# Kernel optimization log

Measured on AMD Instinct MI355X. Metric: run time of the kernel, lower is better.

The kernel has to match this reference:

```python
import math
import jax, jax.numpy as jnp
import numpy as np

EMBED = 256
HEADS = 8
HEAD_DIM = 32
LAYERS = 6
FFN = 1024
CLAMP = 30
EPS = 1e-12


def _layer_norm(x, g, b):
    m = jnp.mean(x, axis=-1, keepdims=True)
    v = jnp.mean(jnp.square(x - m), axis=-1, keepdims=True)
    return (x - m) * jax.lax.rsqrt(v + EPS) * g + b


def setup_inputs() -> dict:
    key = jax.random.key(0)
    ks = jax.random.split(key, 24)
    B, N = 8, 1023
    S = N + 1
    sd = 0.02
    inp = {}
    inp["node_feat"] = jax.random.normal(ks[0], (B, N, 140), jnp.float32)
    inp["node_opcode"] = jax.random.randint(ks[1], (B, N), 0, 120)
    inp["dist_matrix"] = jax.random.randint(ks[2], (B, S, S), 0, 64)
    # node embedder params
    inp["W_op"] = jax.random.normal(ks[3], (120, EMBED), jnp.float32) * sd
    inp["W_feat"] = jax.random.normal(ks[4], (140, EMBED), jnp.float32) * sd
    inp["b_feat"] = jnp.zeros((EMBED,), jnp.float32)
    inp["W_mlp1"] = jax.random.normal(ks[5], (2 * EMBED, EMBED), jnp.float32) * sd
    inp["b_mlp1"] = jnp.zeros((EMBED,), jnp.float32)
    inp["W_mlp2"] = jax.random.normal(ks[6], (EMBED, EMBED), jnp.float32) * sd
    inp["b_mlp2"] = jnp.zeros((EMBED,), jnp.float32)
    inp["cls"] = jax.random.normal(ks[7], (1, 1, EMBED), jnp.float32)
    # distance bias table: mat[i] = e^(-i/sqrt(clamp)) - 1, size clamp+2
    inp["dist_table"] = jnp.asarray(
        [math.e ** (-i / CLAMP ** 0.5) - 1.0 for i in range(CLAMP + 2)], jnp.float32)
    # transformer layer params, stacked over layers
    inp["Wq"] = jax.random.normal(ks[8], (LAYERS, EMBED, EMBED), jnp.float32) * sd
    inp["bq"] = jnp.zeros((LAYERS, EMBED), jnp.float32)
    inp["Wk"] = jax.random.normal(ks[9], (LAYERS, EMBED, EMBED), jnp.float32) * sd
    inp["bk"] = jnp.zeros((LAYERS, EMBED), jnp.float32)
    inp["Wv"] = jax.random.normal(ks[10], (LAYERS, EMBED, EMBED), jnp.float32) * sd
    inp["bv"] = jnp.zeros((LAYERS, EMBED), jnp.float32)
    inp["Wo"] = jax.random.normal(ks[11], (LAYERS, EMBED, EMBED), jnp.float32) * sd
    inp["bo"] = jnp.zeros((LAYERS, EMBED), jnp.float32)
    inp["ln1_g"] = jnp.ones((LAYERS, EMBED), jnp.float32)
    inp["ln1_b"] = jnp.zeros((LAYERS, EMBED), jnp.float32)
    inp["Wf1"] = jax.random.normal(ks[12], (LAYERS, EMBED, FFN), jnp.float32) * sd
    inp["bf1"] = jnp.zeros((LAYERS, FFN), jnp.float32)
    inp["Wf2"] = jax.random.normal(ks[13], (LAYERS, FFN, EMBED), jnp.float32) * sd
    inp["bf2"] = jnp.zeros((LAYERS, EMBED), jnp.float32)
    inp["ln2_g"] = jnp.ones((LAYERS, EMBED), jnp.float32)
    inp["ln2_b"] = jnp.zeros((LAYERS, EMBED), jnp.float32)
    return inp


def reference(node_feat, W_op, W_feat, b_feat, W_mlp1, b_mlp1, W_mlp2, b_mlp2,
              cls, dist_table, Wq, bq, Wk, bk, Wv, bv, Wo, bo, ln1_g, ln1_b,
              Wf1, bf1, Wf2, bf2, ln2_g, ln2_b, node_opcode, dist_matrix):
    B, N, _ = node_feat.shape
    S = N + 1
    # node embedder: [op_emb ; feat_proj] -> Linear -> GELU -> Linear
    op_enc = W_op[node_opcode]                                  # [B,N,E]
    f_enc = node_feat @ W_feat + b_feat                         # [B,N,E]
    h = jnp.concatenate([op_enc, f_enc], axis=-1)               # [B,N,2E]
    h = jax.nn.gelu(h @ W_mlp1 + b_mlp1, approximate=False) @ W_mlp2 + b_mlp2
    x = jnp.concatenate([jnp.broadcast_to(cls, (B, 1, EMBED)), h], axis=1)  # [B,S,E]
    # distance bias: -1 -> clamp+2, >clamp -> clamp+1, then table gather
    d = dist_matrix
    idx = jnp.where(d == -1, CLAMP + 2, jnp.where(d > CLAMP, CLAMP + 1, d))
    bias = dist_table[idx]                                      # [B,S,S]
    bias4 = bias[:, None, :, :]                                 # broadcast over heads
    scale = 1.0 / math.sqrt(HEAD_DIM)

    def split_heads(t):
        return t.reshape(B, S, HEADS, HEAD_DIM).transpose(0, 2, 1, 3)

    for i in range(LAYERS):
        q = split_heads(x @ Wq[i] + bq[i])                      # [B,H,S,Dh]
        k = split_heads(x @ Wk[i] + bk[i])
        v = split_heads(x @ Wv[i] + bv[i])
        scores = jnp.einsum('bhqd,bhkd->bhqk', q, k) * scale + bias4
        attn = jax.nn.softmax(scores, axis=-1)
        ctx = jnp.einsum('bhqk,bhkd->bhqd', attn, v)
        ctx = ctx.transpose(0, 2, 1, 3).reshape(B, S, EMBED)
        x = _layer_norm(x + ctx @ Wo[i] + bo[i], ln1_g[i], ln1_b[i])
        ff = jax.nn.gelu(x @ Wf1[i] + bf1[i], approximate=False) @ Wf2[i] + bf2[i]
        x = _layer_norm(x + ff, ln2_g[i], ln2_b[i])
    return x
```

## Files before the change

### kernel.cpp

```cpp
#include <hip/hip_runtime.h>
#include <math.h>

#define B_ 8
#define N_ 1023
#define S_ 1024
#define E_ 256
#define H_ 8
#define D_ 32
#define L_ 6
#define F_ 1024
#define LDK 72

typedef __attribute__((ext_vector_type(8))) short bf16x8;
typedef __attribute__((ext_vector_type(4))) float f32x4;

__device__ __forceinline__ ushort f2b(float x) {
    unsigned u = __float_as_uint(x);
    return (ushort)((u + 0x7fffu + ((u >> 16) & 1u)) >> 16);
}

__global__ __launch_bounds__(256) void bias_kernel(const int* __restrict__ dm,
                                                   const float* __restrict__ table,
                                                   float* __restrict__ out) {
    int idx = blockIdx.x * 256 + threadIdx.x;
    int d = dm[idx];
    int ii = ((unsigned)d > 30u) ? 31 : d;
    out[idx] = table[ii];
}

__global__ __launch_bounds__(256) void opgather_kernel(const int* __restrict__ opc,
                                                       const float* __restrict__ W_op,
                                                       float* __restrict__ hcat) {
    int idx = blockIdx.x * 256 + threadIdx.x;
    int row = idx >> 8, c = idx & 255;
    hcat[(size_t)row * 512 + c] = W_op[opc[row] * 256 + c];
}

__global__ __launch_bounds__(256) void assemble_kernel(const float* __restrict__ cls,
                                                       const float* __restrict__ h,
                                                       float* __restrict__ x,
                                                       ushort* __restrict__ xb) {
    int idx = blockIdx.x * 256 + threadIdx.x;
    int c = idx & 255;
    int s = (idx >> 8) & 1023;
    int b = idx >> 18;
    float v = (s == 0) ? cls[c] : h[((size_t)(b * N_ + s - 1)) * 256 + c];
    x[idx] = v;
    xb[idx] = f2b(v);
}

__global__ __launch_bounds__(256) void wconv_t(const float* __restrict__ in,
                                               ushort* __restrict__ out,
                                               int K, int Nn) {
    int idx = blockIdx.x * 256 + threadIdx.x;
    int per = K * Nn;
    int lw = idx / per, rem = idx - lw * per;
    int n = rem / K, k = rem - n * K;
    out[idx] = f2b(in[(size_t)lw * per + (size_t)k * Nn + n]);
}

template<int EPI>
__global__ __launch_bounds__(256) void mgemm(
    const ushort* __restrict__ A, const ushort* __restrict__ Bt,
    const float* __restrict__ bias, void* __restrict__ C,
    int M, int Nn, int K)
{
    __shared__ ushort As[64 * 32];
    __shared__ ushort Bs[64 * 32];
    const int t = threadIdx.x;
    const int m0 = blockIdx.x * 64, n0 = blockIdx.y * 64;
    const int l = t & 63, w = t >> 6;
    const int wr = (w >> 1) * 32, wc = (w & 1) * 32;
    const int sr = t >> 2, sc = (t & 3) * 8;
    const int l15 = l & 15, lk = (l >> 4) * 8;

    f32x4 zero = {0.f, 0.f, 0.f, 0.f};
    f32x4 acc00 = zero, acc01 = zero, acc10 = zero, acc11 = zero;

    const ushort* ap = A + (size_t)(m0 + sr) * K + sc;
    const ushort* bp = Bt + (size_t)(n0 + sr) * K + sc;
    bf16x8 ra = *(const bf16x8*)ap;
    bf16x8 rb = *(const bf16x8*)bp;

    for (int kt = 0; kt < K; kt += 32) {
        *(bf16x8*)&As[sr * 32 + sc] = ra;
        *(bf16x8*)&Bs[sr * 32 + sc] = rb;
        __syncthreads();
        if (kt + 32 < K) {
            ra = *(const bf16x8*)(ap + kt + 32);
            rb = *(const bf16x8*)(bp + kt + 32);
        }
        bf16x8 a0 = *(bf16x8*)&As[(wr + l15) * 32 + lk];
        bf16x8 a1 = *(bf16x8*)&As[(wr + 16 + l15) * 32 + lk];
        bf16x8 b0 = *(bf16x8*)&Bs[(wc + l15) * 32 + lk];
        bf16x8 b1 = *(bf16x8*)&Bs[(wc + 16 + l15) * 32 + lk];
        acc00 = __builtin_amdgcn_mfma_f32_16x16x32_bf16(a0, b0, acc00, 0, 0, 0);
        acc01 = __builtin_amdgcn_mfma_f32_16x16x32_bf16(a0, b1, acc01, 0, 0, 0);
        acc10 = __builtin_amdgcn_mfma_f32_16x16x32_bf16(a1, b0, acc10, 0, 0, 0);
        acc11 = __builtin_amdgcn_mfma_f32_16x16x32_bf16(a1, b1, acc11, 0, 0, 0);
        __syncthreads();
    }
    const int cn = n0 + wc + l15;
    const int rbase = m0 + wr + (l >> 4) * 4;
    float bv0 = bias[cn], bv1 = bias[cn + 16];
    #pragma unroll
    for (int i = 0; i < 2; i++) {
        f32x4 aj0 = i ? acc10 : acc00;
        f32x4 aj1 = i ? acc11 : acc01;
        #pragma unroll
        for (int r = 0; r < 4; r++) {
            int row = rbase + i * 16 + r;
            float v0 = aj0[r] + bv0;
            float v1 = aj1[r] + bv1;
            if (EPI == 0) {
                ((float*)C)[(size_t)row * Nn + cn] = v0;
                ((float*)C)[(size_t)row * Nn + cn + 16] = v1;
            } else {
                if (EPI == 1) {
                    v0 = 0.5f * v0 * (1.f + erff(v0 * 0.70710678118654752f));
                    v1 = 0.5f * v1 * (1.f + erff(v1 * 0.70710678118654752f));
                }
                ((ushort*)C)[(size_t)row * Nn + cn] = f2b(v0);
                ((ushort*)C)[(size_t)row * Nn + cn + 16] = f2b(v1);
            }
        }
    }
}

template<int EPI>
__global__ __launch_bounds__(256) void gemm_kernel(
    const float* __restrict__ A, int lda,
    const float* __restrict__ Bm, int ldb,
    const float* __restrict__ bias,
    float* __restrict__ C, int ldc,
    int M, int Nn, int K)
{
    __shared__ float As[16][68];
    __shared__ float Bs[16][68];
    const int t = threadIdx.x;
    const int m0 = blockIdx.x * 64, n0 = blockIdx.y * 64;
    const int tx = t & 15, ty = t >> 4;
    const int tm = ty * 4, tn = tx * 4;
    float acc[4][4] = {};
    const int am = t >> 2, ak = (t & 3) * 4;
    const int bkr = t >> 4, bn4 = (t & 15) * 4;
    const int nt = (K + 15) >> 4;
    for (int kt = 0; kt < nt; kt++) {
        int k0 = kt * 16;
        #pragma unroll
        for (int j = 0; j < 4; j++) {
            int kk = k0 + ak + j;
            float v = 0.f;
            if (m0 + am < M && kk < K) v = A[(size_t)(m0 + am) * lda + kk];
            As[ak + j][am] = v;
        }
        {
            float4 v = {0.f, 0.f, 0.f, 0.f};
            if (k0 + bkr < K) v = *(const float4*)&Bm[(size_t)(k0 + bkr) * ldb + n0 + bn4];
            *(float4*)&Bs[bkr][bn4] = v;
        }
        __syncthreads();
        #pragma unroll
        for (int kk = 0; kk < 16; kk++) {
            float4 a = *(const float4*)&As[kk][tm];
            float4 b = *(const float4*)&Bs[kk][tn];
            float av[4] = {a.x, a.y, a.z, a.w};
            float bw[4] = {b.x, b.y, b.z, b.w};
            #pragma unroll
            for (int i = 0; i < 4; i++)
                #pragma unroll
                for (int j = 0; j < 4; j++)
                    acc[i][j] = fmaf(av[i], bw[j], acc[i][j]);
        }
        __syncthreads();
    }
    #pragma unroll
    for (int j = 0; j < 4; j++) {
        float bv = bias ? bias[n0 + tn + j] : 0.f;
        #pragma unroll
        for (int i = 0; i < 4; i++) {
            int m = m0 + tm + i;
            if (m < M) {
                float v = acc[i][j] + bv;
                if (EPI == 1) v = 0.5f * v * (1.f + erff(v * 0.70710678118654752f));
                C[(size_t)m * ldc + n0 + tn + j] = v;
            }
        }
    }
}

__global__ __launch_bounds__(256, 2) void attn_mfma(
    const ushort* __restrict__ Qm, const ushort* __restrict__ Km,
    const ushort* __restrict__ Vm, const float* __restrict__ bias,
    ushort* __restrict__ ctxb)
{
    __shared__ ushort Vt[32 * LDK];
    __shared__ ushort Pl[4][32 * LDK];
    const int t = threadIdx.x;
    const int bid = blockIdx.x;
    const int qt = bid & 7;
    const int h  = (bid >> 3) & 7;
    const int b  = bid >> 6;
    const int wv = t >> 6, l = t & 63;
    const int g = l >> 4, l15 = l & 15;
    const float scale = 0.17677669529663687f;

    const int q0 = qt * 128 + wv * 32;
    const size_t base = (size_t)(b * S_) * E_ + h * D_;

    bf16x8 qf[2];
    #pragma unroll
    for (int qs = 0; qs < 2; qs++)
        qf[qs] = *(const bf16x8*)&Qm[base + (size_t)(q0 + qs * 16 + l15) * E_ + g * 8];

    f32x4 ctx[2][2] = {};
    float mrun[2] = {-3e38f, -3e38f}, lrun[2] = {0.f, 0.f};

    const int pr = t >> 3, dq = (t & 7) * 4;
    const ushort* vrow0 = &Vm[base + (size_t)(2 * pr) * E_ + dq];
    const float* bp = bias + ((size_t)b * S_ + q0) * S_;
    ushort* pw = &Pl[wv][0];

    for (int kt = 0; kt < S_; kt += 64) {
        ushort4 v0 = *(const ushort4*)&vrow0[(size_t)kt * E_];
        ushort4 v1 = *(const ushort4*)&vrow0[(size_t)kt * E_ + E_];

        f32x4 s[4][2];
        #pragma unroll
        for (int ks = 0; ks < 4; ks++) {
            bf16x8 kf = *(const bf16x8*)&Km[base + (size_t)(kt + ks * 16 + l15) * E_ + g * 8];
            #pragma unroll
            for (int qs = 0; qs < 2; qs++) {
                f32x4 z = {0.f, 0.f, 0.f, 0.f};
                s[ks][qs] = __builtin_amdgcn_mfma_f32_16x16x32_bf16(kf, qf[qs], z, 0, 0, 0);
            }
        }
        #pragma unroll
        for (int qs = 0; qs < 2; qs++) {
            const float* bq_ = bp + (size_t)(qs * 16 + l15) * S_ + kt + g * 4;
            #pragma unroll
            for (int ks = 0; ks < 4; ks++) {
                float4 bb = *(const float4*)&bq_[ks * 16];
                s[ks][qs][0] = fmaf(s[ks][qs][0], scale, bb.x);
                s[ks][qs][1] = fmaf(s[ks][qs][1], scale, bb.y);
                s[ks][qs][2] = fmaf(s[ks][qs][2], scale, bb.z);
                s[ks][qs][3] = fmaf(s[ks][qs][3], scale, bb.w);
            }
        }
        #pragma unroll
        for (int qs = 0; qs < 2; qs++) {
            float mx = s[0][qs][0];
            #pragma unroll
            for (int ks = 0; ks < 4; ks++)
                #pragma unroll
                for (int r = 0; r < 4; r++) mx = fmaxf(mx, s[ks][qs][r]);
            mx = fmaxf(mx, __shfl_xor(mx, 16, 64));
            mx = fmaxf(mx, __shfl_xor(mx, 32, 64));
            float mn = fmaxf(mrun[qs], mx);
            float corr = __expf(mrun[qs] - mn);
            mrun[qs] = mn;
            float ps = 0.f;
            #pragma unroll
            for (int ks = 0; ks < 4; ks++)
                #pragma unroll
                for (int r = 0; r < 4; r++) {
                    float e = __expf(s[ks][qs][r] - mn);
                    s[ks][qs][r] = e; ps += e;
                }
            ps += __shfl_xor(ps, 16, 64);
            ps += __shfl_xor(ps, 32, 64);
            lrun[qs] = lrun[qs] * corr + ps;
            #pragma unroll
            for (int ds = 0; ds < 2; ds++) {
                ctx[ds][qs][0] *= corr; ctx[ds][qs][1] *= corr;
                ctx[ds][qs][2] *= corr; ctx[ds][qs][3] *= corr;
            }
        }
        #pragma unroll
        for (int qs = 0; qs < 2; qs++)
            #pragma unroll
            for (int ks = 0; ks < 4; ks++) {
                uint2 pk;
                pk.x = (uint)f2b(s[ks][qs][0]) | ((uint)f2b(s[ks][qs][1]) << 16);
                pk.y = (uint)f2b(s[ks][qs][2]) | ((uint)f2b(s[ks][qs][3]) << 16);
                *(uint2*)&pw[(qs * 16 + l15) * LDK + ks * 16 + g * 4] = pk;
            }
        __syncthreads();
        {
            uint p0 = (uint)v0.x | ((uint)v1.x << 16);
            uint p1 = (uint)v0.y | ((uint)v1.y << 16);
            uint p2 = (uint)v0.z | ((uint)v1.z << 16);
            uint p3 = (uint)v0.w | ((uint)v1.w << 16);
            *(uint*)&Vt[(dq + 0) * LDK + 2 * pr] = p0;
            *(uint*)&Vt[(dq + 1) * LDK + 2 * pr] = p1;
            *(uint*)&Vt[(dq + 2) * LDK + 2 * pr] = p2;
            *(uint*)&Vt[(dq + 3) * LDK + 2 * pr] = p3;
        }
        __syncthreads();
        #pragma unroll
        for (int kc = 0; kc < 2; kc++) {
            bf16x8 pf[2], vf[2];
            #pragma unroll
            for (int qs = 0; qs < 2; qs++)
                pf[qs] = *(bf16x8*)&pw[(qs * 16 + l15) * LDK + kc * 32 + g * 8];
            #pragma unroll
            for (int ds = 0; ds < 2; ds++)
                vf[ds] = *(bf16x8*)&Vt[(ds * 16 + l15) * LDK + kc * 32 + g * 8];
            #pragma unroll
            for (int ds = 0; ds < 2; ds++)
                #pragma unroll
                for (int qs = 0; qs < 2; qs++)
                    ctx[ds][qs] = __builtin_amdgcn_mfma_f32_16x16x32_bf16(
                        vf[ds], pf[qs], ctx[ds][qs], 0, 0, 0);
        }
    }
    #pragma unroll
    for (int qs = 0; qs < 2; qs++) {
        float inv = 1.f / lrun[qs];
        ushort* op = &ctxb[base + (size_t)(q0 + qs * 16 + l15) * E_];
        #pragma unroll
        for (int ds = 0; ds < 2; ds++)
            #pragma unroll
            for (int r = 0; r < 4; r++)
                op[ds * 16 + g * 4 + r] = f2b(ctx[ds][qs][r] * inv);
    }
}

__global__ __launch_bounds__(64) void ln_kernel(
    const float* __restrict__ xin, const float* __restrict__ add,
    const float* __restrict__ g, const float* __restrict__ bt,
    float* __restrict__ xout, ushort* __restrict__ xbout)
{
    int row = blockIdx.x, t = threadIdx.x;
    float4 xv = *(const float4*)&xin[(size_t)row * E_ + t * 4];
    float4 av = *(const float4*)&add[(size_t)row * E_ + t * 4];
    xv.x += av.x; xv.y += av.y; xv.z += av.z; xv.w += av.w;
    float sum = xv.x + xv.y + xv.z + xv.w;
    #pragma unroll
    for (int off = 32; off; off >>= 1) sum += __shfl_xor(sum, off, 64);
    float mean = sum * (1.f / 256.f);
    float dx = xv.x - mean, dy = xv.y - mean, dz = xv.z - mean, dw = xv.w - mean;
    float sq = dx * dx + dy * dy + dz * dz + dw * dw;
    #pragma unroll
    for (int off = 32; off; off >>= 1) sq += __shfl_xor(sq, off, 64);
    float rstd = rsqrtf(sq * (1.f / 256.f) + 1e-12f);
    float4 gv = *(const float4*)&g[t * 4];
    float4 bv = *(const float4*)&bt[t * 4];
    float4 ov;
    ov.x = dx * rstd * gv.x + bv.x;
    ov.y = dy * rstd * gv.y + bv.y;
    ov.z = dz * rstd * gv.z + bv.z;
    ov.w = dw * rstd * gv.w + bv.w;
    *(float4*)&xout[(size_t)row * E_ + t * 4] = ov;
    ushort4 hb;
    hb.x = f2b(ov.x); hb.y = f2b(ov.y); hb.z = f2b(ov.z); hb.w = f2b(ov.w);
    *(ushort4*)&xbout[(size_t)row * E_ + t * 4] = hb;
}

extern "C" void kernel_launch(void* const* d_in, const int* in_sizes, int n_in,
                              void* d_out, int out_size, void* d_ws, size_t ws_size,
                              hipStream_t stream) {
    const float* node_feat = (const float*)d_in[0];
    const int*   node_opc  = (const int*)d_in[1];
    const int*   dist_mat  = (const int*)d_in[2];
    const float* W_op      = (const float*)d_in[3];
    const float* W_feat    = (const float*)d_in[4];
    const float* b_feat    = (const float*)d_in[5];
    const float* W_mlp1    = (const float*)d_in[6];
    const float* b_mlp1    = (const float*)d_in[7];
    const float* W_mlp2    = (const float*)d_in[8];
    const float* b_mlp2    = (const float*)d_in[9];
    const float* cls       = (const float*)d_in[10];
    const float* dist_tab  = (const float*)d_in[11];
    const float* Wq = (const float*)d_in[12]; const float* bq = (const float*)d_in[13];
    const float* Wk = (const float*)d_in[14]; const float* bk = (const float*)d_in[15];
    const float* Wv = (const float*)d_in[16]; const float* bv = (const float*)d_in[17];
    const float* Wo = (const float*)d_in[18]; const float* bo = (const float*)d_in[19];
    const float* ln1g = (const float*)d_in[20]; const float* ln1b = (const float*)d_in[21];
    const float* Wf1 = (const float*)d_in[22]; const float* bf1 = (const float*)d_in[23];
    const float* Wf2 = (const float*)d_in[24]; const float* bf2 = (const float*)d_in[25];
    const float* ln2g = (const float*)d_in[26]; const float* ln2b = (const float*)d_in[27];

    float* out = (float*)d_out;
    float* ws  = (float*)d_ws;
    float* biasb = ws;
    float* x     = biasb + 8388608;
    float* qb    = x  + 2097152;
    float* kb    = qb + 2097152;
    float* vb    = kb + 2097152;
    float* big   = vb + 2097152;
    float* mlbuf = big + 8388608;
    ushort* xb   = (ushort*)(mlbuf + 524288);
    ushort* cbb  = xb + 2097152;
    ushort* wts  = cbb + 2097152;
    float*  hcat  = big;
    ushort* ffnb  = (ushort*)big;
    float* h1 = qb;
    float* h2 = kb;
    ushort* qbb = (ushort*)qb;
    ushort* kbb = (ushort*)kb;
    ushort* vbb = (ushort*)vb;

    ushort* wqt  = wts;
    ushort* wkt  = wqt + 393216;
    ushort* wvt  = wkt + 393216;
    ushort* wot  = wvt + 393216;
    ushort* wf1t = wot + 393216;
    ushort* wf2t = wf1t + 1572864;

    wconv_t<<<1536, 256, 0, stream>>>(Wq, wqt, 256, 256);
    wconv_t<<<1536, 256, 0, stream>>>(Wk, wkt, 256, 256);
    wconv_t<<<1536, 256, 0, stream>>>(Wv, wvt, 256, 256);
    wconv_t<<<1536, 256, 0, stream>>>(Wo, wot, 256, 256);
    wconv_t<<<6144, 256, 0, stream>>>(Wf1, wf1t, 256, 1024);
    wconv_t<<<6144, 256, 0, stream>>>(Wf2, wf2t, 1024, 256);

    bias_kernel<<<32768, 256, 0, stream>>>(dist_mat, dist_tab, biasb);
    opgather_kernel<<<8184, 256, 0, stream>>>(node_opc, W_op, hcat);
    gemm_kernel<0><<<dim3(128, 4), 256, 0, stream>>>(node_feat, 140, W_feat, 256, b_feat,
                                                     hcat + 256, 512, 8184, 256, 140);
    gemm_kernel<1><<<dim3(128, 4), 256, 0, stream>>>(hcat, 512, W_mlp1, 256, b_mlp1,
                                                     h1, 256, 8184, 256, 512);
    gemm_kernel<0><<<dim3(128, 4), 256, 0, stream>>>(h1, 256, W_mlp2, 256, b_mlp2,
                                                     h2, 256, 8184, 256, 256);
    assemble_kernel<<<8192, 256, 0, stream>>>(cls, h2, x, xb);

    for (int l = 0; l < L_; l++) {
        const ushort* wqt_l = wqt + l * 65536;  const float* bq_l = bq + l * 256;
        const ushort* wkt_l = wkt + l * 65536;  const float* bk_l = bk + l * 256;
        const ushort* wvt_l = wvt + l * 65536;  const float* bv_l = bv + l * 256;
        const ushort* wot_l = wot + l * 65536;  const float* bo_l = bo + l * 256;
        const ushort* wf1t_l = wf1t + l * 262144; const float* bf1_l = bf1 + l * 1024;
        const ushort* wf2t_l = wf2t + l * 262144; const float* bf2_l = bf2 + l * 256;

        mgemm<2><<<dim3(128, 4), 256, 0, stream>>>(xb, wqt_l, bq_l, qbb, 8192, 256, 256);
        mgemm<2><<<dim3(128, 4), 256, 0, stream>>>(xb, wkt_l, bk_l, kbb, 8192, 256, 256);
        mgemm<2><<<dim3(128, 4), 256, 0, stream>>>(xb, wvt_l, bv_l, vbb, 8192, 256, 256);
        attn_mfma<<<512, 256, 0, stream>>>(qbb, kbb, vbb, biasb, cbb);
        mgemm<0><<<dim3(128, 4), 256, 0, stream>>>(cbb, wot_l, bo_l, qb, 8192, 256, 256);
        ln_kernel<<<8192, 64, 0, stream>>>(x, qb, ln1g + l * 256, ln1b + l * 256, x, xb);
        mgemm<1><<<dim3(128, 16), 256, 0, stream>>>(xb, wf1t_l, bf1_l, ffnb, 8192, 1024, 256);
        mgemm<0><<<dim3(128, 4), 256, 0, stream>>>((const ushort*)ffnb, wf2t_l, bf2_l, qb,
                                                   8192, 256, 1024);
        ln_kernel<<<8192, 64, 0, stream>>>(x, qb, ln2g + l * 256, ln2b + l * 256,
                                           (l == L_ - 1) ? out : x, xb);
    }
}
```

Baseline: 978.6 us.

## Enlarge MFMA GEMM tiles and move the embedder GEMMs to bf16 MFMA

The bf16 MFMA GEMM now uses 128-row tiles, with 64- or 128-column tiles, padded shared-memory rows, and 4xN accumulator fragments per wave. This raises data reuse per block and cuts LDS bank conflicts. The three fp32 SIMT embedder GEMMs are replaced by the same MFMA kernel, with node features, the op gather and the MLP weights converted to bf16 and K padded to 160. This removes the slow fp32 FMA path, but the embedder now runs at bf16 precision and the new block count (64x4) gives fewer blocks per GPU.

```diff
diff --git a/kernel.cpp b/kernel.cpp
--- a/kernel.cpp
+++ b/kernel.cpp
@@ -28,12 +28,21 @@
     out[idx] = table[ii];
 }
 
+__global__ __launch_bounds__(256) void nfconv(const float* __restrict__ nf,
+                                              ushort* __restrict__ out) {
+    int idx = blockIdx.x * 256 + threadIdx.x;
+    int r = idx / 160, k = idx - r * 160;
+    float v = (r < 8184 && k < 140) ? nf[r * 140 + k] : 0.f;
+    out[idx] = f2b(v);
+}
+
 __global__ __launch_bounds__(256) void opgather_kernel(const int* __restrict__ opc,
                                                        const float* __restrict__ W_op,
-                                                       float* __restrict__ hcat) {
+                                                       ushort* __restrict__ hcatb) {
     int idx = blockIdx.x * 256 + threadIdx.x;
     int row = idx >> 8, c = idx & 255;
-    hcat[(size_t)row * 512 + c] = W_op[opc[row] * 256 + c];
+    float v = (row < 8184) ? W_op[opc[row] * 256 + c] : 0.f;
+    hcatb[(size_t)row * 512 + c] = f2b(v);
 }
 
 __global__ __launch_bounds__(256) void assemble_kernel(const float* __restrict__ cls,
@@ -51,139 +60,91 @@
 
 __global__ __launch_bounds__(256) void wconv_t(const float* __restrict__ in,
                                                ushort* __restrict__ out,
-                                               int K, int Nn) {
+                                               int K, int Kp, int Nn) {
     int idx = blockIdx.x * 256 + threadIdx.x;
-    int per = K * Nn;
+    int per = Kp * Nn;
     int lw = idx / per, rem = idx - lw * per;
-    int n = rem / K, k = rem - n * K;
-    out[idx] = f2b(in[(size_t)lw * per + (size_t)k * Nn + n]);
-}
-
-template<int EPI>
-__global__ __launch_bounds__(256) void mgemm(
+    int n = rem / Kp, k = rem - n * Kp;
+    out[idx] = (k < K) ? f2b(in[(size_t)lw * K * Nn + (size_t)k * Nn + n]) : (ushort)0;
+}
+
+template<int EPI, int BN>
+__global__ __launch_bounds__(256) void mgemm2(
     const ushort* __restrict__ A, const ushort* __restrict__ Bt,
     const float* __restrict__ bias, void* __restrict__ C,
-    int M, int Nn, int K)
+    int M, int Nn, int K, int ldc)
 {
-    __shared__ ushort As[64 * 32];
-    __shared__ ushort Bs[64 * 32];
+    constexpr int NB = BN / 32;
+    __shared__ ushort As[128 * 36];
+    __shared__ ushort Bs[BN * 36];
     const int t = threadIdx.x;
-    const int m0 = blockIdx.x * 64, n0 = blockIdx.y * 64;
+    const int m0 = blockIdx.x * 128, n0 = blockIdx.y * BN;
     const int l = t & 63, w = t >> 6;
-    const int wr = (w >> 1) * 32, wc = (w & 1) * 32;
-    const int sr = t >> 2, sc = (t & 3) * 8;
-    const int l15 = l & 15, lk = (l >> 4) * 8;
-
-    f32x4 zero = {0.f, 0.f, 0.f, 0.f};
-    f32x4 acc00 = zero, acc01 = zero, acc10 = zero, acc11 = zero;
-
-    const ushort* ap = A + (size_t)(m0 + sr) * K + sc;
-    const ushort* bp = Bt + (size_t)(n0 + sr) * K + sc;
-    bf16x8 ra = *(const bf16x8*)ap;
-    bf16x8 rb = *(const bf16x8*)bp;
+    const int wr = (w >> 1) * 64, wc = (w & 1) * (BN / 2);
+    const int l15 = l & 15, g8 = (l >> 4) * 8;
+
+    const int ar = t >> 1, ac = (t & 1) * 16;
+    const int br = (BN == 128) ? (t >> 1) : (t >> 2);
+    const int bc = (BN == 128) ? ((t & 1) * 16) : ((t & 3) * 8);
+
+    f32x4 acc[4][NB];
+    #pragma unroll
+    for (int i = 0; i < 4; i++)
+        #pragma unroll
+        for (int j = 0; j < NB; j++)
+            acc[i][j] = (f32x4){0.f, 0.f, 0.f, 0.f};
+
+    const ushort* ap = A + (size_t)(m0 + ar) * K + ac;
+    const ushort* bp = Bt + (size_t)(n0 + br) * K + bc;
+    bf16x8 ra0 = *(const bf16x8*)ap;
+    bf16x8 ra1 = *(const bf16x8*)(ap + 8);
+    bf16x8 rb0 = *(const bf16x8*)bp;
+    bf16x8 rb1;
+    if constexpr (BN == 128) rb1 = *(const bf16x8*)(bp + 8);
 
     for (int kt = 0; kt < K; kt += 32) {
-        *(bf16x8*)&As[sr * 32 + sc] = ra;
-        *(bf16x8*)&Bs[sr * 32 + sc] = rb;
+        *(bf16x8*)&As[ar * 36 + ac] = ra0;
+        *(bf16x8*)&As[ar * 36 + ac + 8] = ra1;
+        *(bf16x8*)&Bs[br * 36 + bc] = rb0;
+        if constexpr (BN == 128) *(bf16x8*)&Bs[br * 36 + bc + 8] = rb1;
         __syncthreads();
         if (kt + 32 < K) {
-            ra = *(const bf16x8*)(ap + kt + 32);
-            rb = *(const bf16x8*)(bp + kt + 32);
-        }
-        bf16x8 a0 = *(bf16x8*)&As[(wr + l15) * 32 + lk];
-        bf16x8 a1 = *(bf16x8*)&As[(wr + 16 + l15) * 32 + lk];
-        bf16x8 b0 = *(bf16x8*)&Bs[(wc + l15) * 32 + lk];
-        bf16x8 b1 = *(bf16x8*)&Bs[(wc + 16 + l15) * 32 + lk];
-        acc00 = __builtin_amdgcn_mfma_f32_16x16x32_bf16(a0, b0, acc00, 0, 0, 0);
-        acc01 = __builtin_amdgcn_mfma_f32_16x16x32_bf16(a0, b1, acc01, 0, 0, 0);
-        acc10 = __builtin_amdgcn_mfma_f32_16x16x32_bf16(a1, b0, acc10, 0, 0, 0);
-        acc11 = __builtin_amdgcn_mfma_f32_16x16x32_bf16(a1, b1, acc11, 0, 0, 0);
+            ra0 = *(const bf16x8*)(ap + kt + 32);
+            ra1 = *(const bf16x8*)(ap + kt + 40);
+            rb0 = *(const bf16x8*)(bp + kt + 32);
+            if constexpr (BN == 128) rb1 = *(const bf16x8*)(bp + kt + 40);
+        }
+        bf16x8 af[4], bfr[NB];
+        #pragma unroll
+        for (int i = 0; i < 4; i++)
+            af[i] = *(bf16x8*)&As[(wr + i * 16 + l15) * 36 + g8];
+        #pragma unroll
+        for (int j = 0; j < NB; j++)
+            bfr[j] = *(bf16x8*)&Bs[(wc + j * 16 + l15) * 36 + g8];
+        #pragma unroll
+        for (int i = 0; i < 4; i++)
+            #pragma unroll
+            for (int j = 0; j < NB; j++)
+                acc[i][j] = __builtin_amdgcn_mfma_f32_16x16x32_bf16(af[i], bfr[j], acc[i][j], 0, 0, 0);
         __syncthreads();
     }
-    const int cn = n0 + wc + l15;
-    const int rbase = m0 + wr + (l >> 4) * 4;
-    float bv0 = bias[cn], bv1 = bias[cn + 16];
-    #pragma unroll
-    for (int i = 0; i < 2; i++) {
-        f32x4 aj0 = i ? acc10 : acc00;
-        f32x4 aj1 = i ? acc11 : acc01;
-        #pragma unroll
-        for (int r = 0; r < 4; r++) {
-            int row = rbase + i * 16 + r;
-            float v0 = aj0[r] + bv0;
-            float v1 = aj1[r] + bv1;
-            if (EPI == 0) {
-                ((float*)C)[(size_t)row * Nn + cn] = v0;
-                ((float*)C)[(size_t)row * Nn + cn + 16] = v1;
-            } else {
-                if (EPI == 1) {
-                    v0 = 0.5f * v0 * (1.f + erff(v0 * 0.70710678118654752f));
-                    v1 = 0.5f * v1 * (1.f + erff(v1 * 0.70710678118654752f));
+    const int rb_ = (l >> 4) * 4;
+    #pragma unroll
+    for (int j = 0; j < NB; j++) {
+        int cn = n0 + wc + j * 16 + l15;
+        float bv = bias[cn];
+        #pragma unroll
+        for (int i = 0; i < 4; i++) {
+            #pragma unroll
+            for (int r = 0; r < 4; r++) {
+                int row = m0 + wr + i * 16 + rb_ + r;
+                float v = acc[i][j][r] + bv;
+                if (EPI == 0) {
+                    ((float*)C)[(size_t)row * ldc + cn] = v;
+                } else {
+                    if (EPI == 1) v = 0.5f * v * (1.f + erff(v * 0.70710678118654752f));
+                    ((ushort*)C)[(size_t)row * ldc + cn] = f2b(v);
                 }
-                ((ushort*)C)[(size_t)row * Nn + cn] = f2b(v0);
-                ((ushort*)C)[(size_t)row * Nn + cn + 16] = f2b(v1);
-            }
-        }
-    }
-}
-
-template<int EPI>
-__global__ __launch_bounds__(256) void gemm_kernel(
-    const float* __restrict__ A, int lda,
-    const float* __restrict__ Bm, int ldb,
-    const float* __restrict__ bias,
-    float* __restrict__ C, int ldc,
-    int M, int Nn, int K)
-{
-    __shared__ float As[16][68];
-    __shared__ float Bs[16][68];
-    const int t = threadIdx.x;
-    const int m0 = blockIdx.x * 64, n0 = blockIdx.y * 64;
-    const int tx = t & 15, ty = t >> 4;
-    const int tm = ty * 4, tn = tx * 4;
-    float acc[4][4] = {};
-    const int am = t >> 2, ak = (t & 3) * 4;
-    const int bkr = t >> 4, bn4 = (t & 15) * 4;
-    const int nt = (K + 15) >> 4;
-    for (int kt = 0; kt < nt; kt++) {
-        int k0 = kt * 16;
-        #pragma unroll
-        for (int j = 0; j < 4; j++) {
-            int kk = k0 + ak + j;
-            float v = 0.f;
-            if (m0 + am < M && kk < K) v = A[(size_t)(m0 + am) * lda + kk];
-            As[ak + j][am] = v;
-        }
-        {
-            float4 v = {0.f, 0.f, 0.f, 0.f};
-            if (k0 + bkr < K) v = *(const float4*)&Bm[(size_t)(k0 + bkr) * ldb + n0 + bn4];
-            *(float4*)&Bs[bkr][bn4] = v;
-        }
-        __syncthreads();
-        #pragma unroll
-        for (int kk = 0; kk < 16; kk++) {
-            float4 a = *(const float4*)&As[kk][tm];
-            float4 b = *(const float4*)&Bs[kk][tn];
-            float av[4] = {a.x, a.y, a.z, a.w};
-            float bw[4] = {b.x, b.y, b.z, b.w};
-            #pragma unroll
-            for (int i = 0; i < 4; i++)
-                #pragma unroll
-                for (int j = 0; j < 4; j++)
-                    acc[i][j] = fmaf(av[i], bw[j], acc[i][j]);
-        }
-        __syncthreads();
-    }
-    #pragma unroll
-    for (int j = 0; j < 4; j++) {
-        float bv = bias ? bias[n0 + tn + j] : 0.f;
-        #pragma unroll
-        for (int i = 0; i < 4; i++) {
-            int m = m0 + tm + i;
-            if (m < M) {
-                float v = acc[i][j] + bv;
-                if (EPI == 1) v = 0.5f * v * (1.f + erff(v * 0.70710678118654752f));
-                C[(size_t)m * ldc + n0 + tn + j] = v;
             }
         }
     }
@@ -393,13 +354,14 @@
     ushort* xb   = (ushort*)(mlbuf + 524288);
     ushort* cbb  = xb + 2097152;
     ushort* wts  = cbb + 2097152;
-    float*  hcat  = big;
-    ushort* ffnb  = (ushort*)big;
-    float* h1 = qb;
-    float* h2 = kb;
     ushort* qbb = (ushort*)qb;
     ushort* kbb = (ushort*)kb;
     ushort* vbb = (ushort*)vb;
+    float*  h2f = vb;
+    ushort* nfb   = (ushort*)big;
+    ushort* hcatb = nfb + 1310720;
+    ushort* h1b   = hcatb + 4194304;
+    ushort* ffnb  = (ushort*)big;
 
     ushort* wqt  = wts;
     ushort* wkt  = wqt + 393216;
@@ -407,23 +369,30 @@
     ushort* wot  = wvt + 393216;
     ushort* wf1t = wot + 393216;
     ushort* wf2t = wf1t + 1572864;
-
-    wconv_t<<<1536, 256, 0, stream>>>(Wq, wqt, 256, 256);
-    wconv_t<<<1536, 256, 0, stream>>>(Wk, wkt, 256, 256);
-    wconv_t<<<1536, 256, 0, stream>>>(Wv, wvt, 256, 256);
-    wconv_t<<<1536, 256, 0, stream>>>(Wo, wot, 256, 256);
-    wconv_t<<<6144, 256, 0, stream>>>(Wf1, wf1t, 256, 1024);
-    wconv_t<<<6144, 256, 0, stream>>>(Wf2, wf2t, 1024, 256);
+    ushort* wft  = wf2t + 1572864;
+    ushort* wm1t = wft + 40960;
+    ushort* wm2t = wm1t + 131072;
+
+    wconv_t<<<1536, 256, 0, stream>>>(Wq, wqt, 256, 256, 256);
+    wconv_t<<<1536, 256, 0, stream>>>(Wk, wkt, 256, 256, 256);
+    wconv_t<<<1536, 256, 0, stream>>>(Wv, wvt, 256, 256, 256);
+    wconv_t<<<1536, 256, 0, stream>>>(Wo, wot, 256, 256, 256);
+    wconv_t<<<6144, 256, 0, stream>>>(Wf1, wf1t, 256, 256, 1024);
+    wconv_t<<<6144, 256, 0, stream>>>(Wf2, wf2t, 1024, 1024, 256);
+    wconv_t<<<160,  256, 0, stream>>>(W_feat, wft, 140, 160, 256);
+    wconv_t<<<512,  256, 0, stream>>>(W_mlp1, wm1t, 512, 512, 256);
+    wconv_t<<<256,  256, 0, stream>>>(W_mlp2, wm2t, 256, 256, 256);
 
     bias_kernel<<<32768, 256, 0, stream>>>(dist_mat, dist_tab, biasb);
-    opgather_kernel<<<8184, 256, 0, stream>>>(node_opc, W_op, hcat);
-    gemm_kernel<0><<<dim3(128, 4), 256, 0, stream>>>(node_feat, 140, W_feat, 256, b_feat,
-                                                     hcat + 256, 512, 8184, 256, 140);
-    gemm_kernel<1><<<dim3(128, 4), 256, 0, stream>>>(hcat, 512, W_mlp1, 256, b_mlp1,
-                                                     h1, 256, 8184, 256, 512);
-    gemm_kernel<0><<<dim3(128, 4), 256, 0, stream>>>(h1, 256, W_mlp2, 256, b_mlp2,
-                                                     h2, 256, 8184, 256, 256);
-    assemble_kernel<<<8192, 256, 0, stream>>>(cls, h2, x, xb);
+    nfconv<<<5120, 256, 0, stream>>>(node_feat, nfb);
+    opgather_kernel<<<8192, 256, 0, stream>>>(node_opc, W_op, hcatb);
+    mgemm2<2, 64><<<dim3(64, 4), 256, 0, stream>>>(nfb, wft, b_feat,
+                                                   (void*)(hcatb + 256), 8192, 256, 160, 512);
+    mgemm2<1, 64><<<dim3(64, 4), 256, 0, stream>>>(hcatb, wm1t, b_mlp1,
+                                                   h1b, 8192, 256, 512, 256);
+    mgemm2<0, 64><<<dim3(64, 4), 256, 0, stream>>>(h1b, wm2t, b_mlp2,
+                                                   h2f, 8192, 256, 256, 256);
+    assemble_kernel<<<8192, 256, 0, stream>>>(cls, h2f, x, xb);
 
     for (int l = 0; l < L_; l++) {
         const ushort* wqt_l = wqt + l * 65536;  const float* bq_l = bq + l * 256;
@@ -433,15 +402,15 @@
         const ushort* wf1t_l = wf1t + l * 262144; const float* bf1_l = bf1 + l * 1024;
         const ushort* wf2t_l = wf2t + l * 262144; const float* bf2_l = bf2 + l * 256;
 
-        mgemm<2><<<dim3(128, 4), 256, 0, stream>>>(xb, wqt_l, bq_l, qbb, 8192, 256, 256);
-        mgemm<2><<<dim3(128, 4), 256, 0, stream>>>(xb, wkt_l, bk_l, kbb, 8192, 256, 256);
-        mgemm<2><<<dim3(128, 4), 256, 0, stream>>>(xb, wvt_l, bv_l, vbb, 8192, 256, 256);
+        mgemm2<2, 64><<<dim3(64, 4), 256, 0, stream>>>(xb, wqt_l, bq_l, qbb, 8192, 256, 256, 256);
+        mgemm2<2, 64><<<dim3(64, 4), 256, 0, stream>>>(xb, wkt_l, bk_l, kbb, 8192, 256, 256, 256);
+        mgemm2<2, 64><<<dim3(64, 4), 256, 0, stream>>>(xb, wvt_l, bv_l, vbb, 8192, 256, 256, 256);
         attn_mfma<<<512, 256, 0, stream>>>(qbb, kbb, vbb, biasb, cbb);
-        mgemm<0><<<dim3(128, 4), 256, 0, stream>>>(cbb, wot_l, bo_l, qb, 8192, 256, 256);
+        mgemm2<0, 64><<<dim3(64, 4), 256, 0, stream>>>(cbb, wot_l, bo_l, qb, 8192, 256, 256, 256);
         ln_kernel<<<8192, 64, 0, stream>>>(x, qb, ln1g + l * 256, ln1b + l * 256, x, xb);
-        mgemm<1><<<dim3(128, 16), 256, 0, stream>>>(xb, wf1t_l, bf1_l, ffnb, 8192, 1024, 256);
-        mgemm<0><<<dim3(128, 4), 256, 0, stream>>>((const ushort*)ffnb, wf2t_l, bf2_l, qb,
-                                                   8192, 256, 1024);
+        mgemm2<1, 128><<<dim3(64, 8), 256, 0, stream>>>(xb, wf1t_l, bf1_l, ffnb, 8192, 1024, 256, 1024);
+        mgemm2<0, 64><<<dim3(64, 4), 256, 0, stream>>>((const ushort*)ffnb, wf2t_l, bf2_l, qb,
+                                                       8192, 256, 1024, 256);
         ln_kernel<<<8192, 64, 0, stream>>>(x, qb, ln2g + l * 256, ln2b + l * 256,
                                            (l == L_ - 1) ? out : x, xb);
     }
```

New measurement: 949.3 us. 1.03x faster.
